# Kernel optimization log

Measured on AMD Instinct MI355X. Metric: run time of the kernel, lower is better.

The kernel has to match this reference:

```python
import jax, jax.numpy as jnp
import numpy as np

EMB_DIM = 768
QKV_DIM = 64
NUM_HEAD = 12


def setup_inputs() -> dict:
    key = jax.random.key(0)
    k1, k2, k3 = jax.random.split(key, 3)
    z = jax.random.normal(k1, (16, 1024, EMB_DIM), dtype=jnp.float32)
    U_qkv = jax.random.normal(k2, (NUM_HEAD, 3, EMB_DIM, QKV_DIM), dtype=jnp.float32) * (1.0 / np.sqrt(EMB_DIM))
    U_msa = jax.random.normal(k3, (NUM_HEAD * QKV_DIM, EMB_DIM), dtype=jnp.float32) * (1.0 / np.sqrt(NUM_HEAD * QKV_DIM))
    return {"z": z, "U_qkv": U_qkv, "U_msa": U_msa}


def reference(z, U_qkv, U_msa):
    # z: [b, n, e]; U_qkv: [h, 3, e, d]; U_msa: [h*d, e]
    qkv = jnp.einsum("bne,hked->khbnd", z, U_qkv)  # [3, h, b, n, d]
    q, k, v = qkv[0], qkv[1], qkv[2]               # each [h, b, n, d]
    scale = 1.0 / jnp.sqrt(jnp.asarray(q.shape[-1], dtype=z.dtype))
    logits = jnp.einsum("hbnd,hbmd->hbnm", q, k) * scale  # [h, b, n, n]
    attn = jax.nn.softmax(logits, axis=-1)
    o = jnp.einsum("hbnm,hbmd->bnhd", attn, v)     # [b, n, h, d]
    b, n = o.shape[0], o.shape[1]
    o = o.reshape(b, n, -1)                        # [b, n, h*d]
    return o @ U_msa                               # [b, n, e]
```

## Files before the change

kernel.cpp:

```cpp
#include <hip/hip_runtime.h>
#include <hip/hip_bf16.h>

typedef _Float16 f16x8 __attribute__((ext_vector_type(8)));
typedef _Float16 f16x4 __attribute__((ext_vector_type(4)));
typedef float f32x4 __attribute__((ext_vector_type(4)));

#define MFMA32(a, b, c) __builtin_amdgcn_mfma_f32_16x16x32_f16(a, b, c, 0, 0, 0)
#define MFMA16(a, b, c) __builtin_amdgcn_mfma_f32_16x16x16f16(a, b, c, 0, 0, 0)

__global__ __launch_bounds__(256) void tconv_kernel(
    const float* __restrict__ in, _Float16* __restrict__ out, int R, int C) {
  size_t bat = (size_t)blockIdx.y * R * C;
  int o = blockIdx.x * 256 + threadIdx.x;
  if (o < R * C) {
    int c = o / R, r = o - c * R;
    out[bat + o] = (_Float16)in[bat + (size_t)r * C + c];
  }
}

__global__ __launch_bounds__(256) void cvt16_kernel(
    const float* __restrict__ in, _Float16* __restrict__ out, int n) {
  int i = (blockIdx.x * 256 + threadIdx.x) * 8;
  if (i < n) {
    float4 a = *(const float4*)(in + i);
    float4 b = *(const float4*)(in + i + 4);
    f16x8 cv;
    cv[0] = (_Float16)a.x; cv[1] = (_Float16)a.y;
    cv[2] = (_Float16)a.z; cv[3] = (_Float16)a.w;
    cv[4] = (_Float16)b.x; cv[5] = (_Float16)b.y;
    cv[6] = (_Float16)b.z; cv[7] = (_Float16)b.w;
    *(f16x8*)(out + i) = cv;
  }
}

__global__ __launch_bounds__(256) void qkv_gemm_kernel(
    const _Float16* __restrict__ zh, const _Float16* __restrict__ Ut,
    _Float16* __restrict__ Qf, _Float16* __restrict__ Kf,
    _Float16* __restrict__ Vt) {
  __shared__ _Float16 As[128][72];
  __shared__ _Float16 Bs[128][72];

  const int tid = threadIdx.x;
  const int wv = tid >> 6, lane = tid & 63, quad = lane >> 4, l16 = lane & 15;
  const int m0 = blockIdx.x * 128;
  const int n0 = blockIdx.y * 128;

  f32x4 acc[2][8] = {};

  for (int k0 = 0; k0 < 768; k0 += 64) {
    __syncthreads();
#pragma unroll
    for (int i = 0; i < 4; ++i) {
      int ch = i * 256 + tid;
      int r = ch >> 3, cc = (ch & 7) << 3;
      *(uint4*)&As[r][cc] =
          *(const uint4*)(zh + (size_t)(m0 + r) * 768 + k0 + cc);
      *(uint4*)&Bs[r][cc] =
          *(const uint4*)(Ut + (size_t)(n0 + r) * 768 + k0 + cc);
    }
    __syncthreads();
#pragma unroll
    for (int ks = 0; ks < 2; ++ks) {
      f16x8 af[2], bfr[8];
#pragma unroll
      for (int rt = 0; rt < 2; ++rt)
        af[rt] = *(const f16x8*)&As[wv * 32 + rt * 16 + l16][ks * 32 + quad * 8];
#pragma unroll
      for (int ct = 0; ct < 8; ++ct)
        bfr[ct] = *(const f16x8*)&Bs[ct * 16 + l16][ks * 32 + quad * 8];
#pragma unroll
      for (int rt = 0; rt < 2; ++rt)
#pragma unroll
        for (int ct = 0; ct < 8; ++ct)
          acc[rt][ct] = MFMA32(af[rt], bfr[ct], acc[rt][ct]);
    }
  }

#pragma unroll
  for (int ct = 0; ct < 8; ++ct) {
    const int g = blockIdx.y * 2 + (ct >> 2);
    const int h = g / 3, kk = g - h * 3;
    const int dd = (ct & 3) * 16 + l16;
#pragma unroll
    for (int rt = 0; rt < 2; ++rt) {
#pragma unroll
      for (int r = 0; r < 4; ++r) {
        int m = m0 + wv * 32 + rt * 16 + quad * 4 + r;
        int b = m >> 10, n = m & 1023;
        _Float16 val = (_Float16)acc[rt][ct][r];
        if (kk == 0)
          Qf[(((size_t)h * 16 + b) * 1024 + n) * 64 + dd] = val;
        else if (kk == 1)
          Kf[(((size_t)h * 16 + b) * 1024 + n) * 64 + dd] = val;
        else
          Vt[(((size_t)h * 16 + b) * 64 + dd) * 1024 + n] = val;
      }
    }
  }
}

__global__ __launch_bounds__(256) void attn_kernel(
    const _Float16* __restrict__ Qf, const _Float16* __restrict__ Kf,
    const _Float16* __restrict__ Vt, _Float16* __restrict__ Of) {
  __shared__ _Float16 Ks[64][72];
  __shared__ _Float16 Vs[64][72];

  const int tid = threadIdx.x;
  const int wv = tid >> 6, lane = tid & 63, quad = lane >> 4, l16 = lane & 15;
  const int hb = blockIdx.x;
  const int h = hb >> 4, b = hb & 15;
  const _Float16* Q = Qf + (size_t)hb * 65536;
  const _Float16* K = Kf + (size_t)hb * 65536;
  const _Float16* V = Vt + (size_t)hb * 65536;
  const int q0 = blockIdx.y * 128 + wv * 32;

  const _Float16 cs = (_Float16)0.18033688011112042f;
  f16x8 qfr[2][2];
#pragma unroll
  for (int mi = 0; mi < 2; ++mi) {
    const _Float16* qp = Q + (size_t)(q0 + mi * 16 + l16) * 64 + quad * 8;
    qfr[mi][0] = *(const f16x8*)qp * cs;
    qfr[mi][1] = *(const f16x8*)(qp + 32) * cs;
  }

  const int r0 = tid >> 3, c0 = (tid & 7) << 3;
  const _Float16* Kst = K + (size_t)r0 * 64 + c0;
  const _Float16* Vst = V + (size_t)r0 * 1024 + c0;

  uint4 kreg[2], vreg[2];
#pragma unroll
  for (int i = 0; i < 2; ++i) {
    kreg[i] = *(const uint4*)(Kst + i * 2048);
    vreg[i] = *(const uint4*)(Vst + i * 32768);
  }

  f32x4 o[2][4] = {};
  float lsum[2] = {};

  for (int t = 0; t < 16; ++t) {
#pragma unroll
    for (int i = 0; i < 2; ++i) {
      *(uint4*)&Ks[r0 + i * 32][c0] = kreg[i];
      *(uint4*)&Vs[r0 + i * 32][c0] = vreg[i];
    }
    __syncthreads();
    if (t < 15) {
      int n1 = (t + 1) * 64;
#pragma unroll
      for (int i = 0; i < 2; ++i) {
        kreg[i] = *(const uint4*)(Kst + (size_t)n1 * 64 + i * 2048);
        vreg[i] = *(const uint4*)(Vst + n1 + i * 32768);
      }
    }

    f32x4 st[2][4] = {};
#pragma unroll
    for (int ct = 0; ct < 4; ++ct) {
      f16x8 k0 = *(const f16x8*)&Ks[ct * 16 + l16][quad * 8];
      f16x8 k1 = *(const f16x8*)&Ks[ct * 16 + l16][32 + quad * 8];
#pragma unroll
      for (int mi = 0; mi < 2; ++mi) {
        st[mi][ct] = MFMA32(k0, qfr[mi][0], st[mi][ct]);
        st[mi][ct] = MFMA32(k1, qfr[mi][1], st[mi][ct]);
      }
    }

    f16x4 pa[2][4];
#pragma unroll
    for (int mi = 0; mi < 2; ++mi)
#pragma unroll
      for (int ct = 0; ct < 4; ++ct)
#pragma unroll
        for (int r = 0; r < 4; ++r) {
          float p = __builtin_amdgcn_exp2f(st[mi][ct][r]);
          lsum[mi] += p;
          pa[mi][ct][r] = (_Float16)p;
        }

#pragma unroll
    for (int dt = 0; dt < 4; ++dt) {
#pragma unroll
      for (int kb = 0; kb < 4; ++kb) {
        f16x4 vf = *(const f16x4*)&Vs[dt * 16 + l16][kb * 16 + quad * 4];
#pragma unroll
        for (int mi = 0; mi < 2; ++mi)
          o[mi][dt] = MFMA16(pa[mi][kb], vf, o[mi][dt]);
      }
    }
    __syncthreads();
  }

#pragma unroll
  for (int mi = 0; mi < 2; ++mi) {
    float s = lsum[mi];
    s += __shfl_xor(s, 16, 64);
    s += __shfl_xor(s, 32, 64);
    lsum[mi] = s;
  }

#pragma unroll
  for (int mi = 0; mi < 2; ++mi) {
#pragma unroll
    for (int r = 0; r < 4; ++r) {
      float inv = 1.f / __shfl(lsum[mi], quad * 4 + r, 64);
      int n = q0 + mi * 16 + quad * 4 + r;
#pragma unroll
      for (int dt = 0; dt < 4; ++dt) {
        int dd = dt * 16 + l16;
        Of[((size_t)b * 1024 + n) * 768 + h * 64 + dd] =
            (_Float16)(o[mi][dt][r] * inv);
      }
    }
  }
}

__global__ __launch_bounds__(256) void out_gemm_kernel(
    const _Float16* __restrict__ A, const _Float16* __restrict__ Bt,
    float* __restrict__ Cout) {
  __shared__ _Float16 As[128][72];
  __shared__ _Float16 Bs[128][72];

  const int tid = threadIdx.x;
  const int wv = tid >> 6, lane = tid & 63, quad = lane >> 4, l16 = lane & 15;
  const int m0 = blockIdx.x * 128;
  const int n0 = blockIdx.y * 128;

  f32x4 acc[2][8] = {};

  for (int k0 = 0; k0 < 768; k0 += 64) {
    __syncthreads();
#pragma unroll
    for (int i = 0; i < 4; ++i) {
      int ch = i * 256 + tid;
      int r = ch >> 3, cc = (ch & 7) << 3;
      *(uint4*)&As[r][cc] =
          *(const uint4*)(A + (size_t)(m0 + r) * 768 + k0 + cc);
      *(uint4*)&Bs[r][cc] =
          *(const uint4*)(Bt + (size_t)(n0 + r) * 768 + k0 + cc);
    }
    __syncthreads();
#pragma unroll
    for (int ks = 0; ks < 2; ++ks) {
      f16x8 af[2], bfr[8];
#pragma unroll
      for (int rt = 0; rt < 2; ++rt)
        af[rt] = *(const f16x8*)&As[wv * 32 + rt * 16 + l16][ks * 32 + quad * 8];
#pragma unroll
      for (int ct = 0; ct < 8; ++ct)
        bfr[ct] = *(const f16x8*)&Bs[ct * 16 + l16][ks * 32 + quad * 8];
#pragma unroll
      for (int rt = 0; rt < 2; ++rt)
#pragma unroll
        for (int ct = 0; ct < 8; ++ct)
          acc[rt][ct] = MFMA32(af[rt], bfr[ct], acc[rt][ct]);
    }
  }

#pragma unroll
  for (int rt = 0; rt < 2; ++rt) {
#pragma unroll
    for (int ct = 0; ct < 8; ++ct) {
#pragma unroll
      for (int r = 0; r < 4; ++r) {
        int m = m0 + wv * 32 + rt * 16 + quad * 4 + r;
        int n = n0 + ct * 16 + l16;
        Cout[(size_t)m * 768 + n] = acc[rt][ct][r];
      }
    }
  }
}

extern "C" void kernel_launch(void* const* d_in, const int* in_sizes, int n_in,
                              void* d_out, int out_size, void* d_ws,
                              size_t ws_size, hipStream_t stream) {
  const float* z = (const float*)d_in[0];
  const float* Uqkv = (const float*)d_in[1];
  const float* Umsa = (const float*)d_in[2];

  char* ws = (char*)d_ws;
  _Float16* Ut_qkv = (_Float16*)(ws);
  _Float16* Ut_msa = (_Float16*)(ws + 3538944);
  _Float16* zh = (_Float16*)(ws + 4718592);
  _Float16* Of = zh;
  _Float16* Qf = (_Float16*)(ws + 29884416);
  _Float16* Kf = (_Float16*)(ws + 55050240);
  _Float16* Vt = (_Float16*)(ws + 80216064);

  tconv_kernel<<<dim3(192, 36), 256, 0, stream>>>(Uqkv, Ut_qkv, 768, 64);
  tconv_kernel<<<dim3(2304, 1), 256, 0, stream>>>(Umsa, Ut_msa, 768, 768);
  cvt16_kernel<<<dim3(6144, 1), 256, 0, stream>>>(z, zh, 16384 * 768);

  qkv_gemm_kernel<<<dim3(128, 18), 256, 0, stream>>>(zh, Ut_qkv, Qf, Kf, Vt);
  attn_kernel<<<dim3(192, 8), 256, 0, stream>>>(Qf, Kf, Vt, Of);
  out_gemm_kernel<<<dim3(128, 6), 256, 0, stream>>>(Of, Ut_msa,
                                                    (float*)d_out);
}
```

Measured before the change: 388.6 us.

## Tile weight transposes, swap QKV GEMM grid order, double attention KV tile

Replaces the naive strided weight transpose with a 32x32 shared-memory tiled transpose using vectorized loads and stores. Swaps the QKV GEMM grid so the 18 weight-column blocks vary fastest, letting blocks that share a z tile run together and reuse it in cache. Doubles the attention K/V tile to 128 keys per iteration, halving loop iterations and barriers, at the cost of more shared memory and registers per block, which may lower occupancy.

After: 412.5 us. 6.1% more time.

```diff
diff --git a/kernel.cpp b/kernel.cpp
--- a/kernel.cpp
+++ b/kernel.cpp
@@ -8,14 +8,24 @@
 #define MFMA32(a, b, c) __builtin_amdgcn_mfma_f32_16x16x32_f16(a, b, c, 0, 0, 0)
 #define MFMA16(a, b, c) __builtin_amdgcn_mfma_f32_16x16x16f16(a, b, c, 0, 0, 0)
 
-__global__ __launch_bounds__(256) void tconv_kernel(
-    const float* __restrict__ in, _Float16* __restrict__ out, int R, int C) {
-  size_t bat = (size_t)blockIdx.y * R * C;
-  int o = blockIdx.x * 256 + threadIdx.x;
-  if (o < R * C) {
-    int c = o / R, r = o - c * R;
-    out[bat + o] = (_Float16)in[bat + (size_t)r * C + c];
-  }
+__global__ __launch_bounds__(256) void tconv_tiled_kernel(
+    const float* __restrict__ in, _Float16* __restrict__ out, int R, int C,
+    int tpr ) {
+  __shared__ float tile[32][33];
+  size_t base = (size_t)blockIdx.y * R * C;
+  int tr = blockIdx.x / tpr, tc = blockIdx.x - tr * tpr;
+  int row = threadIdx.x >> 3, c4 = (threadIdx.x & 7) << 2;
+  float4 v =
+      *(const float4*)(in + base + (size_t)(tr * 32 + row) * C + tc * 32 + c4);
+  tile[row][c4 + 0] = v.x;
+  tile[row][c4 + 1] = v.y;
+  tile[row][c4 + 2] = v.z;
+  tile[row][c4 + 3] = v.w;
+  __syncthreads();
+  f16x4 ov;
+#pragma unroll
+  for (int j = 0; j < 4; ++j) ov[j] = (_Float16)tile[c4 + j][row];
+  *(f16x4*)(out + base + (size_t)(tc * 32 + row) * R + tr * 32 + c4) = ov;
 }
 
 __global__ __launch_bounds__(256) void cvt16_kernel(
@@ -42,8 +52,8 @@
 
   const int tid = threadIdx.x;
   const int wv = tid >> 6, lane = tid & 63, quad = lane >> 4, l16 = lane & 15;
-  const int m0 = blockIdx.x * 128;
-  const int n0 = blockIdx.y * 128;
+  const int m0 = blockIdx.y * 128;
+  const int n0 = blockIdx.x * 128;
 
   f32x4 acc[2][8] = {};
 
@@ -78,7 +88,7 @@
 
 #pragma unroll
   for (int ct = 0; ct < 8; ++ct) {
-    const int g = blockIdx.y * 2 + (ct >> 2);
+    const int g = blockIdx.x * 2 + (ct >> 2);
     const int h = g / 3, kk = g - h * 3;
     const int dd = (ct & 3) * 16 + l16;
 #pragma unroll
@@ -102,8 +112,8 @@
 __global__ __launch_bounds__(256) void attn_kernel(
     const _Float16* __restrict__ Qf, const _Float16* __restrict__ Kf,
     const _Float16* __restrict__ Vt, _Float16* __restrict__ Of) {
-  __shared__ _Float16 Ks[64][72];
-  __shared__ _Float16 Vs[64][72];
+  __shared__ _Float16 Ks[128][72];
+  __shared__ _Float16 Vs[64][136];
 
   const int tid = threadIdx.x;
   const int wv = tid >> 6, lane = tid & 63, quad = lane >> 4, l16 = lane & 15;
@@ -123,68 +133,73 @@
     qfr[mi][1] = *(const f16x8*)(qp + 32) * cs;
   }
 
-  const int r0 = tid >> 3, c0 = (tid & 7) << 3;
-  const _Float16* Kst = K + (size_t)r0 * 64 + c0;
-  const _Float16* Vst = V + (size_t)r0 * 1024 + c0;
-
-  uint4 kreg[2], vreg[2];
-#pragma unroll
-  for (int i = 0; i < 2; ++i) {
+  const int kr = tid >> 3, kc = (tid & 7) << 3;
+  const int vr = tid >> 4, vc = (tid & 15) << 3;
+  const _Float16* Kst = K + (size_t)kr * 64 + kc;
+  const _Float16* Vst = V + (size_t)vr * 1024 + vc;
+
+  uint4 kreg[4], vreg[4];
+#pragma unroll
+  for (int i = 0; i < 4; ++i) {
     kreg[i] = *(const uint4*)(Kst + i * 2048);
-    vreg[i] = *(const uint4*)(Vst + i * 32768);
+    vreg[i] = *(const uint4*)(Vst + i * 16384);
   }
 
   f32x4 o[2][4] = {};
   float lsum[2] = {};
 
-  for (int t = 0; t < 16; ++t) {
-#pragma unroll
-    for (int i = 0; i < 2; ++i) {
-      *(uint4*)&Ks[r0 + i * 32][c0] = kreg[i];
-      *(uint4*)&Vs[r0 + i * 32][c0] = vreg[i];
-    }
-    __syncthreads();
-    if (t < 15) {
-      int n1 = (t + 1) * 64;
-#pragma unroll
-      for (int i = 0; i < 2; ++i) {
+  for (int t = 0; t < 8; ++t) {
+#pragma unroll
+    for (int i = 0; i < 4; ++i) {
+      *(uint4*)&Ks[kr + i * 32][kc] = kreg[i];
+      *(uint4*)&Vs[vr + i * 16][vc] = vreg[i];
+    }
+    __syncthreads();
+    if (t < 7) {
+      int n1 = (t + 1) * 128;
+#pragma unroll
+      for (int i = 0; i < 4; ++i) {
         kreg[i] = *(const uint4*)(Kst + (size_t)n1 * 64 + i * 2048);
-        vreg[i] = *(const uint4*)(Vst + n1 + i * 32768);
-      }
-    }
-
-    f32x4 st[2][4] = {};
-#pragma unroll
-    for (int ct = 0; ct < 4; ++ct) {
-      f16x8 k0 = *(const f16x8*)&Ks[ct * 16 + l16][quad * 8];
-      f16x8 k1 = *(const f16x8*)&Ks[ct * 16 + l16][32 + quad * 8];
-#pragma unroll
-      for (int mi = 0; mi < 2; ++mi) {
-        st[mi][ct] = MFMA32(k0, qfr[mi][0], st[mi][ct]);
-        st[mi][ct] = MFMA32(k1, qfr[mi][1], st[mi][ct]);
-      }
-    }
-
-    f16x4 pa[2][4];
-#pragma unroll
-    for (int mi = 0; mi < 2; ++mi)
-#pragma unroll
-      for (int ct = 0; ct < 4; ++ct)
-#pragma unroll
-        for (int r = 0; r < 4; ++r) {
-          float p = __builtin_amdgcn_exp2f(st[mi][ct][r]);
-          lsum[mi] += p;
-          pa[mi][ct][r] = (_Float16)p;
+        vreg[i] = *(const uint4*)(Vst + n1 + i * 16384);
+      }
+    }
+
+#pragma unroll
+    for (int sub = 0; sub < 2; ++sub) {
+      f32x4 st[2][4] = {};
+#pragma unroll
+      for (int ct = 0; ct < 4; ++ct) {
+        f16x8 k0 = *(const f16x8*)&Ks[sub * 64 + ct * 16 + l16][quad * 8];
+        f16x8 k1 = *(const f16x8*)&Ks[sub * 64 + ct * 16 + l16][32 + quad * 8];
+#pragma unroll
+        for (int mi = 0; mi < 2; ++mi) {
+          st[mi][ct] = MFMA32(k0, qfr[mi][0], st[mi][ct]);
+          st[mi][ct] = MFMA32(k1, qfr[mi][1], st[mi][ct]);
         }
-
-#pragma unroll
-    for (int dt = 0; dt < 4; ++dt) {
-#pragma unroll
-      for (int kb = 0; kb < 4; ++kb) {
-        f16x4 vf = *(const f16x4*)&Vs[dt * 16 + l16][kb * 16 + quad * 4];
-#pragma unroll
-        for (int mi = 0; mi < 2; ++mi)
-          o[mi][dt] = MFMA16(pa[mi][kb], vf, o[mi][dt]);
+      }
+
+      f16x4 pa[2][4];
+#pragma unroll
+      for (int mi = 0; mi < 2; ++mi)
+#pragma unroll
+        for (int ct = 0; ct < 4; ++ct)
+#pragma unroll
+          for (int r = 0; r < 4; ++r) {
+            float p = __builtin_amdgcn_exp2f(st[mi][ct][r]);
+            lsum[mi] += p;
+            pa[mi][ct][r] = (_Float16)p;
+          }
+
+#pragma unroll
+      for (int dt = 0; dt < 4; ++dt) {
+#pragma unroll
+        for (int kb = 0; kb < 4; ++kb) {
+          f16x4 vf = *(const f16x4*)&Vs[dt * 16 + l16]
+                                       [sub * 64 + kb * 16 + quad * 4];
+#pragma unroll
+          for (int mi = 0; mi < 2; ++mi)
+            o[mi][dt] = MFMA16(pa[mi][kb], vf, o[mi][dt]);
+        }
       }
     }
     __syncthreads();
@@ -286,11 +301,13 @@
   _Float16* Kf = (_Float16*)(ws + 55050240);
   _Float16* Vt = (_Float16*)(ws + 80216064);
 
-  tconv_kernel<<<dim3(192, 36), 256, 0, stream>>>(Uqkv, Ut_qkv, 768, 64);
-  tconv_kernel<<<dim3(2304, 1), 256, 0, stream>>>(Umsa, Ut_msa, 768, 768);
+  tconv_tiled_kernel<<<dim3(48, 36), 256, 0, stream>>>(Uqkv, Ut_qkv, 768, 64,
+                                                       2);
+  tconv_tiled_kernel<<<dim3(576, 1), 256, 0, stream>>>(Umsa, Ut_msa, 768, 768,
+                                                       24);
   cvt16_kernel<<<dim3(6144, 1), 256, 0, stream>>>(z, zh, 16384 * 768);
 
-  qkv_gemm_kernel<<<dim3(128, 18), 256, 0, stream>>>(zh, Ut_qkv, Qf, Kf, Vt);
+  qkv_gemm_kernel<<<dim3(18, 128), 256, 0, stream>>>(zh, Ut_qkv, Qf, Kf, Vt);
   attn_kernel<<<dim3(192, 8), 256, 0, stream>>>(Qf, Kf, Vt, Of);
   out_gemm_kernel<<<dim3(128, 6), 256, 0, stream>>>(Of, Ut_msa,
                                                     (float*)d_out);
```
